# Kernel optimization log

Hardware: AMD Instinct MI355X
Metric: run time of the kernel (lower is better)

Reference implementation:

```python
import jax, jax.numpy as jnp
import numpy as np

N_SRC, N_TGT, K = 16384, 65536, 8      # coarse nodes, fine nodes, IDW neighbours per target
C, C_SKIP, S, HID = 16, 2, 32, 64      # mv channels (d_model), skip mv channels, scalars, MLP hidden
MV = 16                                # PGA multivector blade dimension


def setup_inputs() -> dict:
    key = jax.random.key(0)
    ks = jax.random.split(key, 11)
    E = N_TGT * K
    return {
        'mv_src': jax.random.normal(ks[0], (N_SRC, C, MV), jnp.float32),
        'mv_skip': jax.random.normal(ks[1], (N_TGT, C_SKIP, MV), jnp.float32),
        'sc_src': jax.random.normal(ks[2], (N_SRC, S), jnp.float32),
        'sc_skip': jax.random.normal(ks[3], (N_TGT, S), jnp.float32),
        'pos_src': jax.random.uniform(ks[4], (N_SRC, 3), jnp.float32),
        'pos_tgt': jax.random.uniform(ks[5], (N_TGT, 3), jnp.float32),
        'interp_source': jax.random.randint(ks[6], (E,), 0, N_SRC, dtype=jnp.int32),
        # every target receives exactly K source contributions (sorted, like torch_geometric knn edges)
        'interp_target': jnp.repeat(jnp.arange(N_TGT, dtype=jnp.int32), K),
        'W1_mv': jax.random.normal(ks[7], (C + C_SKIP, HID), jnp.float32) / np.float32(np.sqrt(C + C_SKIP)),
        'W2_mv': jax.random.normal(ks[8], (HID, C), jnp.float32) / np.float32(np.sqrt(HID)),
        'W1_s': jax.random.normal(ks[9], (2 * S, HID), jnp.float32) / np.float32(np.sqrt(2 * S)),
        'b1_s': jnp.zeros((HID,), jnp.float32),
        'W2_s': jax.random.normal(ks[10], (HID, S), jnp.float32) / np.float32(np.sqrt(HID)),
        'b2_s': jnp.zeros((S,), jnp.float32),
    }


def _interp(mv_src, mv_skip, sc_src, sc_skip, pos_src, pos_tgt,
            interp_source, interp_target, W1_mv, W2_mv, W1_s, b1_s, W2_s, b2_s):
    # --- inverse-distance-weighted interpolation (gather -> weight -> scatter-sum) ---
    pos_diff = pos_src[interp_source] - pos_tgt[interp_target]            # [E,3]
    d2 = jnp.clip(jnp.sum(pos_diff * pos_diff, axis=-1), 1e-16)           # [E]
    w = 1.0 / d2                                                          # IDW weight
    denom = jax.ops.segment_sum(w, interp_target, num_segments=N_TGT)     # [N_tgt]
    mv = jax.ops.segment_sum(mv_src[interp_source] * w[:, None, None],
                             interp_target, num_segments=N_TGT) / denom[:, None, None]
    sc = jax.ops.segment_sum(sc_src[interp_source] * w[:, None],
                             interp_target, num_segments=N_TGT) / denom[:, None]
    # --- skip concat (torch.cat dim=-2 for multivectors, dim=-1 for scalars) ---
    mv = jnp.concatenate((mv, mv_skip), axis=-2)                          # [N_tgt, C+C_SKIP, 16]
    sc = jnp.concatenate((sc, sc_skip), axis=-1)                          # [N_tgt, 2S]
    # --- equivariant MLP: channel-mixing linear on multivectors (blade-wise), gated scalar path ---
    mv_h = jnp.einsum('nci,ch->nhi', mv, W1_mv)                           # [N_tgt, HID, 16]
    sc_h = jax.nn.gelu(sc @ W1_s + b1_s)                                  # [N_tgt, HID]
    mv_o = jnp.einsum('nhi,hc->nci', mv_h, W2_mv)                         # [N_tgt, C, 16]
    sc_o = sc_h @ W2_s + b2_s                                             # [N_tgt, S]
    return mv_o, sc_o


def reference(mv_src, mv_skip, sc_src, sc_skip, pos_src, pos_tgt,
              interp_source, interp_target, W1_mv, W2_mv, W1_s, b1_s, W2_s, b2_s):
    return _interp(mv_src, mv_skip, sc_src, sc_skip, pos_src, pos_tgt,
                   interp_source, interp_target, W1_mv, W2_mv, W1_s, b1_s, W2_s, b2_s)
```

## Files before the change

kernel.cpp:

```cpp
#include <hip/hip_runtime.h>
#include <hip/hip_fp16.h>

#define N_SRC 16384
#define N_TGT 65536
#define KNN 8
#define CMV 16
#define CSKIP 2
#define SSC 32
#define HID 64
#define MVD 16

#define OUT_MV_ELEMS (N_TGT * CMV * MVD)
#define PROJ_OFFSET 512
#define WN_OFFSET (PROJ_OFFSET + (N_SRC * 256 / 2))

typedef float vf4 __attribute__((ext_vector_type(4)));

__device__ __forceinline__ float4 nt_load4(const float* p) {
    vf4 v = __builtin_nontemporal_load((const vf4*)p);
    return make_float4(v.x, v.y, v.z, v.w);
}
__device__ __forceinline__ void nt_store4(float* p, float4 o) {
    vf4 v; v.x = o.x; v.y = o.y; v.z = o.z; v.w = o.w;
    __builtin_nontemporal_store(v, (vf4*)p);
}

__device__ __forceinline__ float gelu_tanh(float x) {
    const float k0 = 0.7978845608028654f;
    const float k1 = 0.044715f;
    float yy = k0 * (x + k1 * x * x * x);
    return 0.5f * x * (1.0f + tanhf(yy));
}

__global__ __launch_bounds__(256) void kA_preproject(
        const float* __restrict__ mv_src,
        const float* __restrict__ pos_src,
        const float* __restrict__ pos_tgt,
        const int*   __restrict__ isrc,
        const float* __restrict__ W1_mv,
        const float* __restrict__ W2_mv,
        float* __restrict__ ws) {
    __shared__ float sWeff[CMV][MVD];
    int tid = threadIdx.x;
    {
        int c = tid >> 4, d = tid & 15;
        float a = 0.f;
        #pragma unroll 8
        for (int h = 0; h < HID; ++h)
            a = fmaf(W1_mv[c * HID + h], W2_mv[h * MVD + d], a);
        sWeff[c][d] = a;
    }
    if (blockIdx.x == 0 && tid < 32) {
        int j = tid >> 4, d = tid & 15;
        float a = 0.f;
        #pragma unroll 8
        for (int h = 0; h < HID; ++h)
            a = fmaf(W1_mv[(CMV + j) * HID + h], W2_mv[h * MVD + d], a);
        ws[j * MVD + d] = a;
    }

    int gid = blockIdx.x * 256 + tid;
    if (gid < N_TGT) {
        int t = gid;
        float ptx = pos_tgt[t * 3 + 0], pty = pos_tgt[t * 3 + 1], ptz = pos_tgt[t * 3 + 2];
        int4 e0 = *(const int4*)(isrc + t * KNN);
        int4 e1 = *(const int4*)(isrc + t * KNN + 4);
        int sk[KNN] = {e0.x, e0.y, e0.z, e0.w, e1.x, e1.y, e1.z, e1.w};
        float wk[KNN];
        float den = 0.f;
        #pragma unroll
        for (int k = 0; k < KNN; ++k) {
            int s = sk[k];
            float dx = pos_src[s * 3 + 0] - ptx;
            float dy = pos_src[s * 3 + 1] - pty;
            float dz = pos_src[s * 3 + 2] - ptz;
            float d2 = fmaxf(dx * dx + dy * dy + dz * dz, 1e-16f);
            wk[k] = 1.0f / d2;
            den += wk[k];
        }
        float invd = 1.0f / den;
        float* wn = ws + WN_OFFSET;
        float4 a = make_float4(wk[0] * invd, wk[1] * invd, wk[2] * invd, wk[3] * invd);
        float4 b = make_float4(wk[4] * invd, wk[5] * invd, wk[6] * invd, wk[7] * invd);
        *(float4*)(wn + (size_t)t * 8)     = a;
        *(float4*)(wn + (size_t)t * 8 + 4) = b;
    }
    __syncthreads();

    int lane = tid & 63;
    int d = lane >> 2, q = lane & 3;
    float wcol[CMV];
    #pragma unroll
    for (int c = 0; c < CMV; ++c) wcol[c] = sWeff[c][d];

    __half* proj = (__half*)(ws + PROJ_OFFSET);
    int wid = (int)((blockIdx.x * blockDim.x + tid) >> 6);
    int nw  = (int)((gridDim.x * blockDim.x) >> 6);
    for (int s = wid; s < N_SRC; s += nw) {
        const float* row = mv_src + (size_t)s * 256;
        float4 o = make_float4(0.f, 0.f, 0.f, 0.f);
        #pragma unroll
        for (int c = 0; c < CMV; ++c) {
            float4 v = *(const float4*)(row + c * 16 + q * 4);
            o.x = fmaf(v.x, wcol[c], o.x);
            o.y = fmaf(v.y, wcol[c], o.y);
            o.z = fmaf(v.z, wcol[c], o.z);
            o.w = fmaf(v.w, wcol[c], o.w);
        }
        union { __half2 h[2]; uint2 u; } P;
        P.h[0] = __floats2half2_rn(o.x, o.y);
        P.h[1] = __floats2half2_rn(o.z, o.w);
        *(uint2*)(proj + (size_t)s * 256 + lane * 4) = P.u;
    }
}

__global__ __launch_bounds__(256, 6) void kB_mv(
        const float* __restrict__ ws,
        const float* __restrict__ mv_skip,
        const int*   __restrict__ isrc,
        float* __restrict__ out) {
    int tid = threadIdx.x;
    int lane = tid & 63;
    int dd = lane >> 2, q = lane & 3;
    float wsk0 = ws[dd], wsk1 = ws[MVD + dd];
    const __half* proj = (const __half*)(ws + PROJ_OFFSET);
    const float*  wn   = ws + WN_OFFSET;

    int wid = (int)((blockIdx.x * blockDim.x + tid) >> 6);
    int t0 = wid * 2;

    int   src2 = 0; float wn2 = 0.f;
    if (lane < 16) {
        src2 = isrc[(size_t)t0 * KNN + lane];
        wn2  = wn[(size_t)t0 * KNN + lane];
    }

    float4 u0A = nt_load4(mv_skip + (size_t)t0 * 32 + q * 4);
    float4 u1A = nt_load4(mv_skip + (size_t)t0 * 32 + 16 + q * 4);
    float4 u0B = nt_load4(mv_skip + (size_t)(t0 + 1) * 32 + q * 4);
    float4 u1B = nt_load4(mv_skip + (size_t)(t0 + 1) * 32 + 16 + q * 4);

    uint2 g[16];
    #pragma unroll
    for (int k = 0; k < 16; ++k) {
        int sk = __builtin_amdgcn_readlane(src2, k);
        g[k] = *(const uint2*)(proj + (size_t)sk * 256 + lane * 4);
    }

    float4 accA = make_float4(0.f, 0.f, 0.f, 0.f);
    float4 accB = make_float4(0.f, 0.f, 0.f, 0.f);
    #pragma unroll
    for (int k = 0; k < KNN; ++k) {
        float wk = __uint_as_float(__builtin_amdgcn_readlane(__float_as_uint(wn2), k));
        union { uint2 u; __half2 h[2]; } P; P.u = g[k];
        float2 lo = __half22float2(P.h[0]);
        float2 hi = __half22float2(P.h[1]);
        accA.x = fmaf(wk, lo.x, accA.x);
        accA.y = fmaf(wk, lo.y, accA.y);
        accA.z = fmaf(wk, hi.x, accA.z);
        accA.w = fmaf(wk, hi.y, accA.w);
    }
    #pragma unroll
    for (int k = 0; k < KNN; ++k) {
        float wk = __uint_as_float(__builtin_amdgcn_readlane(__float_as_uint(wn2), 8 + k));
        union { uint2 u; __half2 h[2]; } P; P.u = g[8 + k];
        float2 lo = __half22float2(P.h[0]);
        float2 hi = __half22float2(P.h[1]);
        accB.x = fmaf(wk, lo.x, accB.x);
        accB.y = fmaf(wk, lo.y, accB.y);
        accB.z = fmaf(wk, hi.x, accB.z);
        accB.w = fmaf(wk, hi.y, accB.w);
    }

    {
        float4 o;
        o.x = accA.x + fmaf(wsk0, u0A.x, wsk1 * u1A.x);
        o.y = accA.y + fmaf(wsk0, u0A.y, wsk1 * u1A.y);
        o.z = accA.z + fmaf(wsk0, u0A.z, wsk1 * u1A.z);
        o.w = accA.w + fmaf(wsk0, u0A.w, wsk1 * u1A.w);
        nt_store4(out + (size_t)t0 * 256 + lane * 4, o);
    }
    {
        float4 o;
        o.x = accB.x + fmaf(wsk0, u0B.x, wsk1 * u1B.x);
        o.y = accB.y + fmaf(wsk0, u0B.y, wsk1 * u1B.y);
        o.z = accB.z + fmaf(wsk0, u0B.z, wsk1 * u1B.z);
        o.w = accB.w + fmaf(wsk0, u0B.w, wsk1 * u1B.w);
        nt_store4(out + (size_t)(t0 + 1) * 256 + lane * 4, o);
    }
}

__global__ __launch_bounds__(256) void kBf_mv(
        const float* __restrict__ mv_src,
        const float* __restrict__ mv_skip,
        const float* __restrict__ pos_src,
        const float* __restrict__ pos_tgt,
        const int*   __restrict__ isrc,
        const float* __restrict__ W1_mv,
        const float* __restrict__ W2_mv,
        float* __restrict__ out) {
    __shared__ float sWeff[CMV + CSKIP][MVD];
    __shared__ float stage[4][256];
    int tid = threadIdx.x;
    for (int e = tid; e < (CMV + CSKIP) * MVD; e += 256) {
        int c = e >> 4, d = e & 15;
        float a = 0.f;
        #pragma unroll 8
        for (int h = 0; h < HID; ++h)
            a = fmaf(W1_mv[c * HID + h], W2_mv[h * MVD + d], a);
        sWeff[c][d] = a;
    }
    __syncthreads();

    int lane = tid & 63, wv = tid >> 6;
    int d = lane >> 2, q = lane & 3;
    float wcol[CMV + CSKIP];
    #pragma unroll
    for (int c = 0; c < CMV + CSKIP; ++c) wcol[c] = sWeff[c][d];

    int wid = (int)((blockIdx.x * blockDim.x + tid) >> 6);
    int nw  = (int)((gridDim.x * blockDim.x) >> 6);
    for (int t = wid; t < N_TGT; t += nw) {
        float w = 0.f; int src = 0;
        if (lane < KNN) {
            src = isrc[t * KNN + lane];
            float dx = pos_src[src * 3 + 0] - pos_tgt[t * 3 + 0];
            float dy = pos_src[src * 3 + 1] - pos_tgt[t * 3 + 1];
            float dz = pos_src[src * 3 + 2] - pos_tgt[t * 3 + 2];
            float d2 = fmaxf(dx * dx + dy * dy + dz * dz, 1e-16f);
            w = 1.0f / d2;
        }
        float denom = w;
        denom += __shfl_xor(denom, 1);
        denom += __shfl_xor(denom, 2);
        denom += __shfl_xor(denom, 4);
        denom = __shfl(denom, 0);
        float invd = 1.0f / denom;

        float4 acc = make_float4(0.f, 0.f, 0.f, 0.f);
        #pragma unroll
        for (int k = 0; k < KNN; ++k) {
            int   sk = __builtin_amdgcn_readlane(src, k);
            float wk = __uint_as_float(__builtin_amdgcn_readlane(__float_as_uint(w), k));
            float4 v = *(const float4*)(mv_src + (size_t)sk * 256 + lane * 4);
            acc.x = fmaf(wk, v.x, acc.x);
            acc.y = fmaf(wk, v.y, acc.y);
            acc.z = fmaf(wk, v.z, acc.z);
            acc.w = fmaf(wk, v.w, acc.w);
        }
        asm volatile("" ::: "memory");
        *(float4*)&stage[wv][lane * 4] = acc;
        asm volatile("s_waitcnt lgkmcnt(0)" ::: "memory");
        __builtin_amdgcn_sched_barrier(0);

        float4 o = make_float4(0.f, 0.f, 0.f, 0.f);
        #pragma unroll
        for (int c = 0; c < CMV; ++c) {
            float4 v = *(const float4*)&stage[wv][c * 16 + q * 4];
            o.x = fmaf(v.x, wcol[c], o.x);
            o.y = fmaf(v.y, wcol[c], o.y);
            o.z = fmaf(v.z, wcol[c], o.z);
            o.w = fmaf(v.w, wcol[c], o.w);
        }
        const float4 u0 = *(const float4*)(mv_skip + (size_t)t * 32 + q * 4);
        const float4 u1 = *(const float4*)(mv_skip + (size_t)t * 32 + 16 + q * 4);
        float4 r;
        r.x = fmaf(o.x, invd, fmaf(wcol[16], u0.x, wcol[17] * u1.x));
        r.y = fmaf(o.y, invd, fmaf(wcol[16], u0.y, wcol[17] * u1.y));
        r.z = fmaf(o.z, invd, fmaf(wcol[16], u0.z, wcol[17] * u1.z));
        r.w = fmaf(o.w, invd, fmaf(wcol[16], u0.w, wcol[17] * u1.w));
        *(float4*)(out + (size_t)t * 256 + lane * 4) = r;
    }
}

__global__ __launch_bounds__(256) void kC_scalar(
        const float* __restrict__ sc_src,
        const float* __restrict__ sc_skip,
        const float* __restrict__ pos_src,
        const float* __restrict__ pos_tgt,
        const int*   __restrict__ isrc,
        const float* __restrict__ wn,
        const float* __restrict__ W1_s,
        const float* __restrict__ b1_s,
        const float* __restrict__ W2_s,
        const float* __restrict__ b2_s,
        float* __restrict__ out) {
    __shared__ float sW1[HID * HID];
    __shared__ float sW2T[SSC][68];
    __shared__ float sXT[HID][68];
    __shared__ float sH[64][68];
    __shared__ float swgt[64][9];
    __shared__ int   ssrcl[64][9];
    __shared__ float sb1[HID], sb2[SSC];

    int tid = threadIdx.x;
    #pragma unroll
    for (int r = 0; r < 4; ++r) {
        float4 v = *(const float4*)(W1_s + (r * 256 + tid) * 4);
        *(float4*)&sW1[(r * 256 + tid) * 4] = v;
    }
    for (int e = tid; e < HID * SSC; e += 256) {
        int h = e >> 5, s = e & 31;
        sW2T[s][h] = W2_s[e];
    }
    if (tid < HID) sb1[tid] = b1_s[tid];
    else if (tid < HID + SSC) sb2[tid - HID] = b2_s[tid - HID];

    int t0 = blockIdx.x * 64;
    if (tid < 64) {
        int t = t0 + tid;
        int4 e0 = *(const int4*)(isrc + t * KNN);
        int4 e1 = *(const int4*)(isrc + t * KNN + 4);
        int sk[KNN] = {e0.x, e0.y, e0.z, e0.w, e1.x, e1.y, e1.z, e1.w};
        float wkn[KNN];
        if (wn) {
            float4 a = *(const float4*)(wn + (size_t)t * 8);
            float4 b = *(const float4*)(wn + (size_t)t * 8 + 4);
            wkn[0] = a.x; wkn[1] = a.y; wkn[2] = a.z; wkn[3] = a.w;
            wkn[4] = b.x; wkn[5] = b.y; wkn[6] = b.z; wkn[7] = b.w;
        } else {
            float ptx = pos_tgt[t * 3 + 0], pty = pos_tgt[t * 3 + 1], ptz = pos_tgt[t * 3 + 2];
            float den = 0.f;
            #pragma unroll
            for (int k = 0; k < KNN; ++k) {
                int s = sk[k];
                float dx = pos_src[s * 3 + 0] - ptx;
                float dy = pos_src[s * 3 + 1] - pty;
                float dz = pos_src[s * 3 + 2] - ptz;
                float d2 = fmaxf(dx * dx + dy * dy + dz * dz, 1e-16f);
                wkn[k] = 1.0f / d2;
                den += wkn[k];
            }
            float invd = 1.0f / den;
            #pragma unroll
            for (int k = 0; k < KNN; ++k) wkn[k] *= invd;
        }
        #pragma unroll
        for (int k = 0; k < KNN; ++k) {
            swgt[tid][k]  = wkn[k];
            ssrcl[tid][k] = sk[k];
        }
    }
    __syncthreads();

    {
        int wv = tid >> 6, lane = tid & 63;
        int k = lane >> 3;
        int m = lane & 7;
        for (int i = 0; i < 16; i += 4) {
            int tb = wv * 16 + i;
            float4 v[4]; float wn4[4];
            #pragma unroll
            for (int j = 0; j < 4; ++j) {
                int tl = tb + j;
                wn4[j] = swgt[tl][k];
                int sk = ssrcl[tl][k];
                v[j] = *(const float4*)(sc_src + (size_t)sk * SSC + m * 4);
            }
            float4 u;
            if (lane < 32)
                u = *(const float4*)(sc_skip + (size_t)(t0 + tb + k) * SSC + m * 4);
            #pragma unroll
            for (int j = 0; j < 4; ++j) {
                float4 a = v[j]; float wnj = wn4[j];
                a.x *= wnj; a.y *= wnj; a.z *= wnj; a.w *= wnj;
                #pragma unroll
                for (int sft = 8; sft <= 32; sft <<= 1) {
                    a.x += __shfl_xor(a.x, sft);
                    a.y += __shfl_xor(a.y, sft);
                    a.z += __shfl_xor(a.z, sft);
                    a.w += __shfl_xor(a.w, sft);
                }
                if (lane < 8) {
                    sXT[4 * lane + 0][tb + j] = a.x;
                    sXT[4 * lane + 1][tb + j] = a.y;
                    sXT[4 * lane + 2][tb + j] = a.z;
                    sXT[4 * lane + 3][tb + j] = a.w;
                }
            }
            if (lane < 32) {
                sXT[SSC + 4 * m + 0][tb + k] = u.x;
                sXT[SSC + 4 * m + 1][tb + k] = u.y;
                sXT[SSC + 4 * m + 2][tb + k] = u.z;
                sXT[SSC + 4 * m + 3][tb + k] = u.w;
            }
        }
    }
    __syncthreads();

    int wv = tid >> 6;
    int lane = tid & 63;
    int tr4 = lane >> 4;
    int hc  = lane & 15;
    int tbase = wv * 16 + tr4 * 4;
    float acc[4][4];
    #pragma unroll
    for (int i = 0; i < 4; ++i)
        #pragma unroll
        for (int j = 0; j < 4; ++j) acc[i][j] = 0.f;

    #pragma unroll 2
    for (int c = 0; c < HID; ++c) {
        float4 xv = *(const float4*)&sXT[c][tbase];
        float4 wv4 = *(const float4*)&sW1[c * HID + hc * 4];
        acc[0][0] = fmaf(xv.x, wv4.x, acc[0][0]);
        acc[0][1] = fmaf(xv.x, wv4.y, acc[0][1]);
        acc[0][2] = fmaf(xv.x, wv4.z, acc[0][2]);
        acc[0][3] = fmaf(xv.x, wv4.w, acc[0][3]);
        acc[1][0] = fmaf(xv.y, wv4.x, acc[1][0]);
        acc[1][1] = fmaf(xv.y, wv4.y, acc[1][1]);
        acc[1][2] = fmaf(xv.y, wv4.z, acc[1][2]);
        acc[1][3] = fmaf(xv.y, wv4.w, acc[1][3]);
        acc[2][0] = fmaf(xv.z, wv4.x, acc[2][0]);
        acc[2][1] = fmaf(xv.z, wv4.y, acc[2][1]);
        acc[2][2] = fmaf(xv.z, wv4.z, acc[2][2]);
        acc[2][3] = fmaf(xv.z, wv4.w, acc[2][3]);
        acc[3][0] = fmaf(xv.w, wv4.x, acc[3][0]);
        acc[3][1] = fmaf(xv.w, wv4.y, acc[3][1]);
        acc[3][2] = fmaf(xv.w, wv4.z, acc[3][2]);
        acc[3][3] = fmaf(xv.w, wv4.w, acc[3][3]);
    }
    {
        float b0 = sb1[hc * 4 + 0], b1 = sb1[hc * 4 + 1];
        float b2 = sb1[hc * 4 + 2], b3 = sb1[hc * 4 + 3];
        #pragma unroll
        for (int i = 0; i < 4; ++i) {
            float4 hv;
            hv.x = gelu_tanh(acc[i][0] + b0);
            hv.y = gelu_tanh(acc[i][1] + b1);
            hv.z = gelu_tanh(acc[i][2] + b2);
            hv.w = gelu_tanh(acc[i][3] + b3);
            *(float4*)&sH[tbase + i][hc * 4] = hv;
        }
    }
    __syncthreads();

    int sc16 = lane & 15;
    float acc2[4][2];
    #pragma unroll
    for (int i = 0; i < 4; ++i) { acc2[i][0] = 0.f; acc2[i][1] = 0.f; }
    #pragma unroll 2
    for (int hh = 0; hh < 16; ++hh) {
        float4 wa = *(const float4*)&sW2T[sc16 * 2 + 0][hh * 4];
        float4 wb = *(const float4*)&sW2T[sc16 * 2 + 1][hh * 4];
        #pragma unroll
        for (int i = 0; i < 4; ++i) {
            float4 hv = *(const float4*)&sH[tbase + i][hh * 4];
            acc2[i][0] = fmaf(hv.x, wa.x, acc2[i][0]);
            acc2[i][0] = fmaf(hv.y, wa.y, acc2[i][0]);
            acc2[i][0] = fmaf(hv.z, wa.z, acc2[i][0]);
            acc2[i][0] = fmaf(hv.w, wa.w, acc2[i][0]);
            acc2[i][1] = fmaf(hv.x, wb.x, acc2[i][1]);
            acc2[i][1] = fmaf(hv.y, wb.y, acc2[i][1]);
            acc2[i][1] = fmaf(hv.z, wb.z, acc2[i][1]);
            acc2[i][1] = fmaf(hv.w, wb.w, acc2[i][1]);
        }
    }
    float* osc = out + OUT_MV_ELEMS;
    float bb0 = sb2[sc16 * 2 + 0], bb1 = sb2[sc16 * 2 + 1];
    #pragma unroll
    for (int i = 0; i < 4; ++i) {
        int t = t0 + tbase + i;
        float2 r = make_float2(acc2[i][0] + bb0, acc2[i][1] + bb1);
        *(float2*)&osc[(size_t)t * SSC + sc16 * 2] = r;
    }
}

extern "C" void kernel_launch(void* const* d_in, const int* in_sizes, int n_in,
                              void* d_out, int out_size, void* d_ws, size_t ws_size,
                              hipStream_t stream) {
    const float* mv_src   = (const float*)d_in[0];
    const float* mv_skip  = (const float*)d_in[1];
    const float* sc_src   = (const float*)d_in[2];
    const float* sc_skip  = (const float*)d_in[3];
    const float* pos_src  = (const float*)d_in[4];
    const float* pos_tgt  = (const float*)d_in[5];
    const int*   isrc     = (const int*)d_in[6];
    const float* W1_mv    = (const float*)d_in[8];
    const float* W2_mv    = (const float*)d_in[9];
    const float* W1_s     = (const float*)d_in[10];
    const float* b1_s     = (const float*)d_in[11];
    const float* W2_s     = (const float*)d_in[12];
    const float* b2_s     = (const float*)d_in[13];
    float* out = (float*)d_out;
    float* ws  = (float*)d_ws;

    size_t need_ws_bytes = (size_t)(WN_OFFSET + (size_t)N_TGT * KNN) * sizeof(float);
    if (ws_size >= need_ws_bytes) {
        hipLaunchKernelGGL(kA_preproject, dim3(512), dim3(256), 0, stream,
                           mv_src, pos_src, pos_tgt, isrc, W1_mv, W2_mv, ws);
        hipLaunchKernelGGL(kB_mv, dim3(8192), dim3(256), 0, stream,
                           ws, mv_skip, isrc, out);
        hipLaunchKernelGGL(kC_scalar, dim3(N_TGT / 64), dim3(256), 0, stream,
                           sc_src, sc_skip, pos_src, pos_tgt, isrc, ws + WN_OFFSET,
                           W1_s, b1_s, W2_s, b2_s, out);
    } else {
        hipLaunchKernelGGL(kBf_mv, dim3(2048), dim3(256), 0, stream,
                           mv_src, mv_skip, pos_src, pos_tgt, isrc, W1_mv, W2_mv, out);
        hipLaunchKernelGGL(kC_scalar, dim3(N_TGT / 64), dim3(256), 0, stream,
                           sc_src, sc_skip, pos_src, pos_tgt, isrc, (const float*)nullptr,
                           W1_s, b1_s, W2_s, b2_s, out);
    }
}
```

Baseline: 201.0 us.

## Fuse multivector gather and scalar MLP into one interleaved kernel launch

Merges the multivector gather kernel and the scalar MLP kernel into a single launch. Every fifth block runs the scalar path and the rest run the multivector path, so the memory-bound gather work and the compute-heavier MLP share the GPU concurrently and one launch boundary goes away. The scalar path is also rewritten per wavefront: each wave handles 8 targets, gathers neighbour rows with shuffles and xor-reductions, and reads W1_s straight from global memory instead of staging it in LDS. The cost is extra shared memory and register pressure in the fused kernel, which could lower occupancy for the multivector blocks.

```diff
diff --git a/kernel.cpp b/kernel.cpp
--- a/kernel.cpp
+++ b/kernel.cpp
@@ -114,79 +114,183 @@
     }
 }
 
-__global__ __launch_bounds__(256, 6) void kB_mv(
+__global__ __launch_bounds__(256, 6) void kFused(
         const float* __restrict__ ws,
         const float* __restrict__ mv_skip,
+        const float* __restrict__ sc_src,
+        const float* __restrict__ sc_skip,
         const int*   __restrict__ isrc,
+        const float* __restrict__ W1_s,
+        const float* __restrict__ b1_s,
+        const float* __restrict__ W2_s,
+        const float* __restrict__ b2_s,
         float* __restrict__ out) {
+    __shared__ float sW2T[SSC][HID + 4];
+    __shared__ float sX[4][8][HID];
+
     int tid = threadIdx.x;
-    int lane = tid & 63;
-    int dd = lane >> 2, q = lane & 3;
-    float wsk0 = ws[dd], wsk1 = ws[MVD + dd];
-    const __half* proj = (const __half*)(ws + PROJ_OFFSET);
-    const float*  wn   = ws + WN_OFFSET;
-
-    int wid = (int)((blockIdx.x * blockDim.x + tid) >> 6);
-    int t0 = wid * 2;
-
-    int   src2 = 0; float wn2 = 0.f;
-    if (lane < 16) {
-        src2 = isrc[(size_t)t0 * KNN + lane];
-        wn2  = wn[(size_t)t0 * KNN + lane];
-    }
-
-    float4 u0A = nt_load4(mv_skip + (size_t)t0 * 32 + q * 4);
-    float4 u1A = nt_load4(mv_skip + (size_t)t0 * 32 + 16 + q * 4);
-    float4 u0B = nt_load4(mv_skip + (size_t)(t0 + 1) * 32 + q * 4);
-    float4 u1B = nt_load4(mv_skip + (size_t)(t0 + 1) * 32 + 16 + q * 4);
-
-    uint2 g[16];
-    #pragma unroll
-    for (int k = 0; k < 16; ++k) {
-        int sk = __builtin_amdgcn_readlane(src2, k);
-        g[k] = *(const uint2*)(proj + (size_t)sk * 256 + lane * 4);
-    }
-
-    float4 accA = make_float4(0.f, 0.f, 0.f, 0.f);
-    float4 accB = make_float4(0.f, 0.f, 0.f, 0.f);
-    #pragma unroll
-    for (int k = 0; k < KNN; ++k) {
-        float wk = __uint_as_float(__builtin_amdgcn_readlane(__float_as_uint(wn2), k));
-        union { uint2 u; __half2 h[2]; } P; P.u = g[k];
-        float2 lo = __half22float2(P.h[0]);
-        float2 hi = __half22float2(P.h[1]);
-        accA.x = fmaf(wk, lo.x, accA.x);
-        accA.y = fmaf(wk, lo.y, accA.y);
-        accA.z = fmaf(wk, hi.x, accA.z);
-        accA.w = fmaf(wk, hi.y, accA.w);
-    }
-    #pragma unroll
-    for (int k = 0; k < KNN; ++k) {
-        float wk = __uint_as_float(__builtin_amdgcn_readlane(__float_as_uint(wn2), 8 + k));
-        union { uint2 u; __half2 h[2]; } P; P.u = g[8 + k];
-        float2 lo = __half22float2(P.h[0]);
-        float2 hi = __half22float2(P.h[1]);
-        accB.x = fmaf(wk, lo.x, accB.x);
-        accB.y = fmaf(wk, lo.y, accB.y);
-        accB.z = fmaf(wk, hi.x, accB.z);
-        accB.w = fmaf(wk, hi.y, accB.w);
-    }
-
+    int bid = blockIdx.x;
+    int lane = tid & 63, wv = tid >> 6;
+    bool is_sc = (bid % 5) == 4;
+
+    if (!is_sc) {
+        int dd = lane >> 2, q = lane & 3;
+        float wsk0 = ws[dd], wsk1 = ws[MVD + dd];
+        const __half* proj = (const __half*)(ws + PROJ_OFFSET);
+        const float*  wn   = ws + WN_OFFSET;
+
+        int mvb = (bid / 5) * 4 + (bid % 5);
+        int wid = mvb * 4 + wv;
+        int t0 = wid * 2;
+
+        int   src2 = 0; float wn2 = 0.f;
+        if (lane < 16) {
+            src2 = isrc[(size_t)t0 * KNN + lane];
+            wn2  = wn[(size_t)t0 * KNN + lane];
+        }
+
+        float4 u0A = nt_load4(mv_skip + (size_t)t0 * 32 + q * 4);
+        float4 u1A = nt_load4(mv_skip + (size_t)t0 * 32 + 16 + q * 4);
+        float4 u0B = nt_load4(mv_skip + (size_t)(t0 + 1) * 32 + q * 4);
+        float4 u1B = nt_load4(mv_skip + (size_t)(t0 + 1) * 32 + 16 + q * 4);
+
+        uint2 g[16];
+        #pragma unroll
+        for (int k = 0; k < 16; ++k) {
+            int sk = __builtin_amdgcn_readlane(src2, k);
+            g[k] = *(const uint2*)(proj + (size_t)sk * 256 + lane * 4);
+        }
+
+        float4 accA = make_float4(0.f, 0.f, 0.f, 0.f);
+        float4 accB = make_float4(0.f, 0.f, 0.f, 0.f);
+        #pragma unroll
+        for (int k = 0; k < KNN; ++k) {
+            float wk = __uint_as_float(__builtin_amdgcn_readlane(__float_as_uint(wn2), k));
+            union { uint2 u; __half2 h[2]; } P; P.u = g[k];
+            float2 lo = __half22float2(P.h[0]);
+            float2 hi = __half22float2(P.h[1]);
+            accA.x = fmaf(wk, lo.x, accA.x);
+            accA.y = fmaf(wk, lo.y, accA.y);
+            accA.z = fmaf(wk, hi.x, accA.z);
+            accA.w = fmaf(wk, hi.y, accA.w);
+        }
+        #pragma unroll
+        for (int k = 0; k < KNN; ++k) {
+            float wk = __uint_as_float(__builtin_amdgcn_readlane(__float_as_uint(wn2), 8 + k));
+            union { uint2 u; __half2 h[2]; } P; P.u = g[8 + k];
+            float2 lo = __half22float2(P.h[0]);
+            float2 hi = __half22float2(P.h[1]);
+            accB.x = fmaf(wk, lo.x, accB.x);
+            accB.y = fmaf(wk, lo.y, accB.y);
+            accB.z = fmaf(wk, hi.x, accB.z);
+            accB.w = fmaf(wk, hi.y, accB.w);
+        }
+
+        {
+            float4 o;
+            o.x = accA.x + fmaf(wsk0, u0A.x, wsk1 * u1A.x);
+            o.y = accA.y + fmaf(wsk0, u0A.y, wsk1 * u1A.y);
+            o.z = accA.z + fmaf(wsk0, u0A.z, wsk1 * u1A.z);
+            o.w = accA.w + fmaf(wsk0, u0A.w, wsk1 * u1A.w);
+            nt_store4(out + (size_t)t0 * 256 + lane * 4, o);
+        }
+        {
+            float4 o;
+            o.x = accB.x + fmaf(wsk0, u0B.x, wsk1 * u1B.x);
+            o.y = accB.y + fmaf(wsk0, u0B.y, wsk1 * u1B.y);
+            o.z = accB.z + fmaf(wsk0, u0B.z, wsk1 * u1B.z);
+            o.w = accB.w + fmaf(wsk0, u0B.w, wsk1 * u1B.w);
+            nt_store4(out + (size_t)(t0 + 1) * 256 + lane * 4, o);
+        }
+        return;
+    }
+
+    for (int e = tid; e < HID * SSC; e += 256) {
+        int h = e >> 5, s = e & 31;
+        sW2T[s][h] = W2_s[e];
+    }
+    __syncthreads();
+
+    const float* wn = ws + WN_OFFSET;
+    int sbid = bid / 5;
+    int t0 = (sbid * 4 + wv) * 8;
+
+    int   se = isrc[(size_t)t0 * KNN + lane];
+    float we = wn[(size_t)t0 * KNN + lane];
+
+    int kk = lane >> 3, mm = lane & 7;
+
+    #pragma unroll
+    for (int tt = 0; tt < 8; ++tt) {
+        int   s = __shfl(se, tt * 8 + kk);
+        float w = __shfl(we, tt * 8 + kk);
+        float4 v = *(const float4*)(sc_src + (size_t)s * SSC + mm * 4);
+        v.x *= w; v.y *= w; v.z *= w; v.w *= w;
+        #pragma unroll
+        for (int sft = 8; sft <= 32; sft <<= 1) {
+            v.x += __shfl_xor(v.x, sft);
+            v.y += __shfl_xor(v.y, sft);
+            v.z += __shfl_xor(v.z, sft);
+            v.w += __shfl_xor(v.w, sft);
+        }
+        if (lane < 8)
+            *(float4*)&sX[wv][tt][lane * 4] = v;
+    }
     {
-        float4 o;
-        o.x = accA.x + fmaf(wsk0, u0A.x, wsk1 * u1A.x);
-        o.y = accA.y + fmaf(wsk0, u0A.y, wsk1 * u1A.y);
-        o.z = accA.z + fmaf(wsk0, u0A.z, wsk1 * u1A.z);
-        o.w = accA.w + fmaf(wsk0, u0A.w, wsk1 * u1A.w);
-        nt_store4(out + (size_t)t0 * 256 + lane * 4, o);
+        int tt = lane >> 3;
+        float4 u = nt_load4(sc_skip + (size_t)(t0 + tt) * SSC + mm * 4);
+        *(float4*)&sX[wv][tt][SSC + mm * 4] = u;
+    }
+
+    float acc1[8];
+    #pragma unroll
+    for (int tt = 0; tt < 8; ++tt) acc1[tt] = 0.f;
+    #pragma unroll 4
+    for (int c4 = 0; c4 < 16; ++c4) {
+        float w0 = W1_s[(c4 * 4 + 0) * HID + lane];
+        float w1 = W1_s[(c4 * 4 + 1) * HID + lane];
+        float w2 = W1_s[(c4 * 4 + 2) * HID + lane];
+        float w3 = W1_s[(c4 * 4 + 3) * HID + lane];
+        #pragma unroll
+        for (int tt = 0; tt < 8; ++tt) {
+            float4 x4 = *(const float4*)&sX[wv][tt][c4 * 4];
+            acc1[tt] = fmaf(x4.x, w0, acc1[tt]);
+            acc1[tt] = fmaf(x4.y, w1, acc1[tt]);
+            acc1[tt] = fmaf(x4.z, w2, acc1[tt]);
+            acc1[tt] = fmaf(x4.w, w3, acc1[tt]);
+        }
     }
     {
-        float4 o;
-        o.x = accB.x + fmaf(wsk0, u0B.x, wsk1 * u1B.x);
-        o.y = accB.y + fmaf(wsk0, u0B.y, wsk1 * u1B.y);
-        o.z = accB.z + fmaf(wsk0, u0B.z, wsk1 * u1B.z);
-        o.w = accB.w + fmaf(wsk0, u0B.w, wsk1 * u1B.w);
-        nt_store4(out + (size_t)(t0 + 1) * 256 + lane * 4, o);
+        float bb = b1_s[lane];
+        #pragma unroll
+        for (int tt = 0; tt < 8; ++tt)
+            sX[wv][tt][lane] = gelu_tanh(acc1[tt] + bb);
+    }
+
+    {
+        int s = lane & 31, th = lane >> 5;
+        float acc2[4];
+        #pragma unroll
+        for (int i = 0; i < 4; ++i) acc2[i] = 0.f;
+        #pragma unroll 4
+        for (int h4 = 0; h4 < 16; ++h4) {
+            float4 w4 = *(const float4*)&sW2T[s][h4 * 4];
+            #pragma unroll
+            for (int i = 0; i < 4; ++i) {
+                float4 x4 = *(const float4*)&sX[wv][th * 4 + i][h4 * 4];
+                acc2[i] = fmaf(x4.x, w4.x, acc2[i]);
+                acc2[i] = fmaf(x4.y, w4.y, acc2[i]);
+                acc2[i] = fmaf(x4.z, w4.z, acc2[i]);
+                acc2[i] = fmaf(x4.w, w4.w, acc2[i]);
+            }
+        }
+        float* osc = out + OUT_MV_ELEMS;
+        float bo = b2_s[s];
+        #pragma unroll
+        for (int i = 0; i < 4; ++i) {
+            int t = t0 + th * 4 + i;
+            __builtin_nontemporal_store(acc2[i] + bo, &osc[(size_t)t * SSC + s]);
+        }
     }
 }
 
@@ -279,7 +383,6 @@
         const float* __restrict__ pos_src,
         const float* __restrict__ pos_tgt,
         const int*   __restrict__ isrc,
-        const float* __restrict__ wn,
         const float* __restrict__ W1_s,
         const float* __restrict__ b1_s,
         const float* __restrict__ W2_s,
@@ -313,31 +416,22 @@
         int4 e1 = *(const int4*)(isrc + t * KNN + 4);
         int sk[KNN] = {e0.x, e0.y, e0.z, e0.w, e1.x, e1.y, e1.z, e1.w};
         float wkn[KNN];
-        if (wn) {
-            float4 a = *(const float4*)(wn + (size_t)t * 8);
-            float4 b = *(const float4*)(wn + (size_t)t * 8 + 4);
-            wkn[0] = a.x; wkn[1] = a.y; wkn[2] = a.z; wkn[3] = a.w;
-            wkn[4] = b.x; wkn[5] = b.y; wkn[6] = b.z; wkn[7] = b.w;
-        } else {
-            float ptx = pos_tgt[t * 3 + 0], pty = pos_tgt[t * 3 + 1], ptz = pos_tgt[t * 3 + 2];
-            float den = 0.f;
-            #pragma unroll
-            for (int k = 0; k < KNN; ++k) {
-                int s = sk[k];
-                float dx = pos_src[s * 3 + 0] - ptx;
-                float dy = pos_src[s * 3 + 1] - pty;
-                float dz = pos_src[s * 3 + 2] - ptz;
-                float d2 = fmaxf(dx * dx + dy * dy + dz * dz, 1e-16f);
-                wkn[k] = 1.0f / d2;
-                den += wkn[k];
-            }
-            float invd = 1.0f / den;
-            #pragma unroll
-            for (int k = 0; k < KNN; ++k) wkn[k] *= invd;
-        }
+        float ptx = pos_tgt[t * 3 + 0], pty = pos_tgt[t * 3 + 1], ptz = pos_tgt[t * 3 + 2];
+        float den = 0.f;
         #pragma unroll
         for (int k = 0; k < KNN; ++k) {
-            swgt[tid][k]  = wkn[k];
+            int s = sk[k];
+            float dx = pos_src[s * 3 + 0] - ptx;
+            float dy = pos_src[s * 3 + 1] - pty;
+            float dz = pos_src[s * 3 + 2] - ptz;
+            float d2 = fmaxf(dx * dx + dy * dy + dz * dz, 1e-16f);
+            wkn[k] = 1.0f / d2;
+            den += wkn[k];
+        }
+        float invd = 1.0f / den;
+        #pragma unroll
+        for (int k = 0; k < KNN; ++k) {
+            swgt[tid][k]  = wkn[k] * invd;
             ssrcl[tid][k] = sk[k];
         }
     }
@@ -489,16 +583,14 @@
     if (ws_size >= need_ws_bytes) {
         hipLaunchKernelGGL(kA_preproject, dim3(512), dim3(256), 0, stream,
                            mv_src, pos_src, pos_tgt, isrc, W1_mv, W2_mv, ws);
-        hipLaunchKernelGGL(kB_mv, dim3(8192), dim3(256), 0, stream,
-                           ws, mv_skip, isrc, out);
-        hipLaunchKernelGGL(kC_scalar, dim3(N_TGT / 64), dim3(256), 0, stream,
-                           sc_src, sc_skip, pos_src, pos_tgt, isrc, ws + WN_OFFSET,
+        hipLaunchKernelGGL(kFused, dim3(10240), dim3(256), 0, stream,
+                           ws, mv_skip, sc_src, sc_skip, isrc,
                            W1_s, b1_s, W2_s, b2_s, out);
     } else {
         hipLaunchKernelGGL(kBf_mv, dim3(2048), dim3(256), 0, stream,
                            mv_src, mv_skip, pos_src, pos_tgt, isrc, W1_mv, W2_mv, out);
         hipLaunchKernelGGL(kC_scalar, dim3(N_TGT / 64), dim3(256), 0, stream,
-                           sc_src, sc_skip, pos_src, pos_tgt, isrc, (const float*)nullptr,
+                           sc_src, sc_skip, pos_src, pos_tgt, isrc,
                            W1_s, b1_s, W2_s, b2_s, out);
     }
 }
```

Result: no change. 199.6 us (-0.7%).

## Pre-project scalar path through W1_s and fuse scalar MLP into mv kernel

Applied to the files above, without the earlier changes.

Because the interpolation is linear, the scalar path now projects sc_src and sc_skip through W1_s (plus bias) ahead of time and stores both in fp16 workspace. The fused kernel gathers the projected 64-wide hidden rows with the same IDW weights, applies GELU, and runs the second layer from LDS. This replaces the separate scalar kernel, which gathered raw 32-wide sc_src rows and did the full first-layer matmul per target. The costs are extra precompute traffic (writing HSK for all targets), fp16 rounding of the hidden activations, and a larger gather per edge (64 vs 32 values, in half precision).

```diff
diff --git a/kernel.cpp b/kernel.cpp
--- a/kernel.cpp
+++ b/kernel.cpp
@@ -12,7 +12,10 @@
 
 #define OUT_MV_ELEMS (N_TGT * CMV * MVD)
 #define PROJ_OFFSET 512
-#define WN_OFFSET (PROJ_OFFSET + (N_SRC * 256 / 2))
+#define WN_OFFSET   (PROJ_OFFSET + (N_SRC * 256 / 2))
+#define P1_OFFSET   (WN_OFFSET + N_TGT * KNN)
+#define HSK_OFFSET  (P1_OFFSET + (N_SRC * HID / 2))
+#define WS_END      (HSK_OFFSET + (N_TGT * HID / 2))
 
 typedef float vf4 __attribute__((ext_vector_type(4)));
 
@@ -32,13 +35,22 @@
     return 0.5f * x * (1.0f + tanhf(yy));
 }
 
+__device__ __forceinline__ float h2f(unsigned short u) {
+    __half h = __ushort_as_half(u);
+    return __half2float(h);
+}
+
 __global__ __launch_bounds__(256) void kA_preproject(
         const float* __restrict__ mv_src,
+        const float* __restrict__ sc_src,
+        const float* __restrict__ sc_skip,
         const float* __restrict__ pos_src,
         const float* __restrict__ pos_tgt,
         const int*   __restrict__ isrc,
         const float* __restrict__ W1_mv,
         const float* __restrict__ W2_mv,
+        const float* __restrict__ W1_s,
+        const float* __restrict__ b1_s,
         float* __restrict__ ws) {
     __shared__ float sWeff[CMV][MVD];
     int tid = threadIdx.x;
@@ -59,9 +71,9 @@
         ws[j * MVD + d] = a;
     }
 
-    int gid = blockIdx.x * 256 + tid;
-    if (gid < N_TGT) {
-        int t = gid;
+    int nthreads = gridDim.x * 256;
+
+    for (int t = blockIdx.x * 256 + tid; t < N_TGT; t += nthreads) {
         float ptx = pos_tgt[t * 3 + 0], pty = pos_tgt[t * 3 + 1], ptz = pos_tgt[t * 3 + 2];
         int4 e0 = *(const int4*)(isrc + t * KNN);
         int4 e1 = *(const int4*)(isrc + t * KNN + 4);
@@ -88,43 +100,82 @@
     __syncthreads();
 
     int lane = tid & 63;
-    int d = lane >> 2, q = lane & 3;
-    float wcol[CMV];
-    #pragma unroll
-    for (int c = 0; c < CMV; ++c) wcol[c] = sWeff[c][d];
-
-    __half* proj = (__half*)(ws + PROJ_OFFSET);
-    int wid = (int)((blockIdx.x * blockDim.x + tid) >> 6);
-    int nw  = (int)((gridDim.x * blockDim.x) >> 6);
-    for (int s = wid; s < N_SRC; s += nw) {
-        const float* row = mv_src + (size_t)s * 256;
-        float4 o = make_float4(0.f, 0.f, 0.f, 0.f);
-        #pragma unroll
-        for (int c = 0; c < CMV; ++c) {
-            float4 v = *(const float4*)(row + c * 16 + q * 4);
-            o.x = fmaf(v.x, wcol[c], o.x);
-            o.y = fmaf(v.y, wcol[c], o.y);
-            o.z = fmaf(v.z, wcol[c], o.z);
-            o.w = fmaf(v.w, wcol[c], o.w);
-        }
-        union { __half2 h[2]; uint2 u; } P;
-        P.h[0] = __floats2half2_rn(o.x, o.y);
-        P.h[1] = __floats2half2_rn(o.z, o.w);
-        *(uint2*)(proj + (size_t)s * 256 + lane * 4) = P.u;
-    }
-}
-
-__global__ __launch_bounds__(256, 6) void kB_mv(
+    int wid = (int)((blockIdx.x * 256 + tid) >> 6);
+    int nw  = nthreads >> 6;
+
+    {
+        int d = lane >> 2, q = lane & 3;
+        float wcol[CMV];
+        #pragma unroll
+        for (int c = 0; c < CMV; ++c) wcol[c] = sWeff[c][d];
+        __half* proj = (__half*)(ws + PROJ_OFFSET);
+        for (int s = wid; s < N_SRC; s += nw) {
+            const float* row = mv_src + (size_t)s * 256;
+            float4 o = make_float4(0.f, 0.f, 0.f, 0.f);
+            #pragma unroll
+            for (int c = 0; c < CMV; ++c) {
+                float4 v = *(const float4*)(row + c * 16 + q * 4);
+                o.x = fmaf(v.x, wcol[c], o.x);
+                o.y = fmaf(v.y, wcol[c], o.y);
+                o.z = fmaf(v.z, wcol[c], o.z);
+                o.w = fmaf(v.w, wcol[c], o.w);
+            }
+            union { __half2 h[2]; uint2 u; } P;
+            P.h[0] = __floats2half2_rn(o.x, o.y);
+            P.h[1] = __floats2half2_rn(o.z, o.w);
+            *(uint2*)(proj + (size_t)s * 256 + lane * 4) = P.u;
+        }
+    }
+
+    {
+        unsigned short* P1 = (unsigned short*)(ws + P1_OFFSET);
+        for (int s = wid; s < N_SRC; s += nw) {
+            float a = 0.f;
+            #pragma unroll 8
+            for (int c = 0; c < SSC; ++c)
+                a = fmaf(sc_src[(size_t)s * SSC + c], W1_s[c * HID + lane], a);
+            P1[(size_t)s * HID + lane] = __half_as_ushort(__float2half_rn(a));
+        }
+    }
+
+    {
+        unsigned short* HSK = (unsigned short*)(ws + HSK_OFFSET);
+        for (int t = wid; t < N_TGT; t += nw) {
+            float a = b1_s[lane];
+            #pragma unroll 8
+            for (int c = 0; c < SSC; ++c)
+                a = fmaf(sc_skip[(size_t)t * SSC + c], W1_s[(SSC + c) * HID + lane], a);
+            HSK[(size_t)t * HID + lane] = __half_as_ushort(__float2half_rn(a));
+        }
+    }
+}
+
+__global__ __launch_bounds__(256, 5) void kFused(
         const float* __restrict__ ws,
         const float* __restrict__ mv_skip,
         const int*   __restrict__ isrc,
+        const float* __restrict__ W2_s,
+        const float* __restrict__ b2_s,
         float* __restrict__ out) {
+    __shared__ float sW2T[SSC][65];
+    __shared__ float sb2[SSC];
+    __shared__ float sH[4][2][HID];
+
     int tid = threadIdx.x;
-    int lane = tid & 63;
+    for (int e = tid; e < HID * SSC; e += 256) {
+        int h = e >> 5, s = e & 31;
+        sW2T[s][h] = W2_s[e];
+    }
+    if (tid < SSC) sb2[tid] = b2_s[tid];
+    __syncthreads();
+
+    int lane = tid & 63, wv = tid >> 6;
     int dd = lane >> 2, q = lane & 3;
     float wsk0 = ws[dd], wsk1 = ws[MVD + dd];
     const __half* proj = (const __half*)(ws + PROJ_OFFSET);
     const float*  wn   = ws + WN_OFFSET;
+    const unsigned short* P1  = (const unsigned short*)(ws + P1_OFFSET);
+    const unsigned short* HSK = (const unsigned short*)(ws + HSK_OFFSET);
 
     int wid = (int)((blockIdx.x * blockDim.x + tid) >> 6);
     int t0 = wid * 2;
@@ -139,12 +190,16 @@
     float4 u1A = nt_load4(mv_skip + (size_t)t0 * 32 + 16 + q * 4);
     float4 u0B = nt_load4(mv_skip + (size_t)(t0 + 1) * 32 + q * 4);
     float4 u1B = nt_load4(mv_skip + (size_t)(t0 + 1) * 32 + 16 + q * 4);
+    unsigned short hsA = HSK[(size_t)t0 * HID + lane];
+    unsigned short hsB = HSK[(size_t)(t0 + 1) * HID + lane];
 
     uint2 g[16];
+    unsigned short p[16];
     #pragma unroll
     for (int k = 0; k < 16; ++k) {
         int sk = __builtin_amdgcn_readlane(src2, k);
         g[k] = *(const uint2*)(proj + (size_t)sk * 256 + lane * 4);
+        p[k] = P1[(size_t)sk * HID + lane];
     }
 
     float4 accA = make_float4(0.f, 0.f, 0.f, 0.f);
@@ -171,7 +226,6 @@
         accB.z = fmaf(wk, hi.x, accB.z);
         accB.w = fmaf(wk, hi.y, accB.w);
     }
-
     {
         float4 o;
         o.x = accA.x + fmaf(wsk0, u0A.x, wsk1 * u1A.x);
@@ -187,6 +241,38 @@
         o.z = accB.z + fmaf(wsk0, u0B.z, wsk1 * u1B.z);
         o.w = accB.w + fmaf(wsk0, u0B.w, wsk1 * u1B.w);
         nt_store4(out + (size_t)(t0 + 1) * 256 + lane * 4, o);
+    }
+
+    float hA = h2f(hsA), hB = h2f(hsB);
+    #pragma unroll
+    for (int k = 0; k < KNN; ++k) {
+        float wkA = __uint_as_float(__builtin_amdgcn_readlane(__float_as_uint(wn2), k));
+        float wkB = __uint_as_float(__builtin_amdgcn_readlane(__float_as_uint(wn2), 8 + k));
+        hA = fmaf(wkA, h2f(p[k]),     hA);
+        hB = fmaf(wkB, h2f(p[8 + k]), hB);
+    }
+    hA = gelu_tanh(hA);
+    hB = gelu_tanh(hB);
+
+    sH[wv][0][lane] = hA;
+    sH[wv][1][lane] = hB;
+    asm volatile("s_waitcnt lgkmcnt(0)" ::: "memory");
+    __builtin_amdgcn_sched_barrier(0);
+
+    {
+        int s = lane & 31, th = lane >> 5;
+        float acc2 = 0.f;
+        #pragma unroll 4
+        for (int h4 = 0; h4 < 16; ++h4) {
+            float4 hv = *(const float4*)&sH[wv][th][h4 * 4];
+            float4 w4 = *(const float4*)&sW2T[s][h4 * 4];
+            acc2 = fmaf(hv.x, w4.x, acc2);
+            acc2 = fmaf(hv.y, w4.y, acc2);
+            acc2 = fmaf(hv.z, w4.z, acc2);
+            acc2 = fmaf(hv.w, w4.w, acc2);
+        }
+        float* osc = out + OUT_MV_ELEMS;
+        __builtin_nontemporal_store(acc2 + sb2[s], &osc[(size_t)(t0 + th) * SSC + s]);
     }
 }
 
@@ -279,7 +365,6 @@
         const float* __restrict__ pos_src,
         const float* __restrict__ pos_tgt,
         const int*   __restrict__ isrc,
-        const float* __restrict__ wn,
         const float* __restrict__ W1_s,
         const float* __restrict__ b1_s,
         const float* __restrict__ W2_s,
@@ -313,31 +398,22 @@
         int4 e1 = *(const int4*)(isrc + t * KNN + 4);
         int sk[KNN] = {e0.x, e0.y, e0.z, e0.w, e1.x, e1.y, e1.z, e1.w};
         float wkn[KNN];
-        if (wn) {
-            float4 a = *(const float4*)(wn + (size_t)t * 8);
-            float4 b = *(const float4*)(wn + (size_t)t * 8 + 4);
-            wkn[0] = a.x; wkn[1] = a.y; wkn[2] = a.z; wkn[3] = a.w;
-            wkn[4] = b.x; wkn[5] = b.y; wkn[6] = b.z; wkn[7] = b.w;
-        } else {
-            float ptx = pos_tgt[t * 3 + 0], pty = pos_tgt[t * 3 + 1], ptz = pos_tgt[t * 3 + 2];
-            float den = 0.f;
-            #pragma unroll
-            for (int k = 0; k < KNN; ++k) {
-                int s = sk[k];
-                float dx = pos_src[s * 3 + 0] - ptx;
-                float dy = pos_src[s * 3 + 1] - pty;
-                float dz = pos_src[s * 3 + 2] - ptz;
-                float d2 = fmaxf(dx * dx + dy * dy + dz * dz, 1e-16f);
-                wkn[k] = 1.0f / d2;
-                den += wkn[k];
-            }
-            float invd = 1.0f / den;
-            #pragma unroll
-            for (int k = 0; k < KNN; ++k) wkn[k] *= invd;
-        }
+        float ptx = pos_tgt[t * 3 + 0], pty = pos_tgt[t * 3 + 1], ptz = pos_tgt[t * 3 + 2];
+        float den = 0.f;
         #pragma unroll
         for (int k = 0; k < KNN; ++k) {
-            swgt[tid][k]  = wkn[k];
+            int s = sk[k];
+            float dx = pos_src[s * 3 + 0] - ptx;
+            float dy = pos_src[s * 3 + 1] - pty;
+            float dz = pos_src[s * 3 + 2] - ptz;
+            float d2 = fmaxf(dx * dx + dy * dy + dz * dz, 1e-16f);
+            wkn[k] = 1.0f / d2;
+            den += wkn[k];
+        }
+        float invd = 1.0f / den;
+        #pragma unroll
+        for (int k = 0; k < KNN; ++k) {
+            swgt[tid][k]  = wkn[k] * invd;
             ssrcl[tid][k] = sk[k];
         }
     }
@@ -485,20 +561,18 @@
     float* out = (float*)d_out;
     float* ws  = (float*)d_ws;
 
-    size_t need_ws_bytes = (size_t)(WN_OFFSET + (size_t)N_TGT * KNN) * sizeof(float);
+    size_t need_ws_bytes = (size_t)WS_END * sizeof(float);
     if (ws_size >= need_ws_bytes) {
-        hipLaunchKernelGGL(kA_preproject, dim3(512), dim3(256), 0, stream,
-                           mv_src, pos_src, pos_tgt, isrc, W1_mv, W2_mv, ws);
-        hipLaunchKernelGGL(kB_mv, dim3(8192), dim3(256), 0, stream,
-                           ws, mv_skip, isrc, out);
-        hipLaunchKernelGGL(kC_scalar, dim3(N_TGT / 64), dim3(256), 0, stream,
-                           sc_src, sc_skip, pos_src, pos_tgt, isrc, ws + WN_OFFSET,
-                           W1_s, b1_s, W2_s, b2_s, out);
+        hipLaunchKernelGGL(kA_preproject, dim3(2048), dim3(256), 0, stream,
+                           mv_src, sc_src, sc_skip, pos_src, pos_tgt, isrc,
+                           W1_mv, W2_mv, W1_s, b1_s, ws);
+        hipLaunchKernelGGL(kFused, dim3(8192), dim3(256), 0, stream,
+                           ws, mv_skip, isrc, W2_s, b2_s, out);
     } else {
         hipLaunchKernelGGL(kBf_mv, dim3(2048), dim3(256), 0, stream,
                            mv_src, mv_skip, pos_src, pos_tgt, isrc, W1_mv, W2_mv, out);
         hipLaunchKernelGGL(kC_scalar, dim3(N_TGT / 64), dim3(256), 0, stream,
-                           sc_src, sc_skip, pos_src, pos_tgt, isrc, (const float*)nullptr,
+                           sc_src, sc_skip, pos_src, pos_tgt, isrc,
                            W1_s, b1_s, W2_s, b2_s, out);
     }
 }
```

Result: slower. 224.8 us (+11.8%).
